# Optimization experiments

Measured on AMD Instinct MI355X. Metric: run time of the kernel, lower is better.

Reference implementation:

```python
import jax, jax.numpy as jnp
import numpy as np

N = 100000      # nodes
E = 1600000     # edges (avg degree 16)
G = 1000        # graphs in batch
F_IN = 128      # num_features
C = 10          # num_classes
EPS = 1e-5


def setup_inputs() -> dict:
    key = jax.random.key(0)
    ks = jax.random.split(key, 12)
    w = lambda k, shape: jax.random.normal(k, shape, jnp.float32) * 0.05
    return {
        'x': jax.random.normal(ks[0], (N, F_IN), jnp.float32),
        'edge_index': jax.random.randint(ks[1], (2, E), 0, N, jnp.int32),
        'edge_weights': jax.random.randint(ks[2], (E,), 0, 2, jnp.int32),
        'batch': jnp.sort(jax.random.randint(ks[3], (N,), 0, G, jnp.int32)),
        'num_graphs': G,
        # initial MLP: Linear(128,32)+BN+ReLU, Linear(32,32)+BN+ReLU
        'W1': w(ks[4], (F_IN, 32)), 'b1': jnp.zeros(32), 'g1': jnp.ones(32), 'bt1': jnp.zeros(32),
        'W2': w(ks[5], (32, 32)), 'b2': jnp.zeros(32), 'g2': jnp.ones(32), 'bt2': jnp.zeros(32),
        'Wl0': w(ks[6], (32, C)), 'bl0': jnp.zeros(C),   # initial_linear
        'Wg1': w(ks[7], (32, 64)), 'bg1': jnp.zeros(64),  # GCNConv 1
        'Wl1': w(ks[8], (64, C)), 'bl1': jnp.zeros(C),
        'Wg2': w(ks[9], (64, 64)), 'bg2': jnp.zeros(64),  # GCNConv 2
        'Wl2': w(ks[10], (64, C)), 'bl2': jnp.zeros(C),
    }


def _bn(h, gamma, beta):
    # BatchNorm1d in training mode: biased batch statistics over nodes
    mu = h.mean(0)
    var = ((h - mu) ** 2).mean(0)
    return gamma * (h - mu) * jax.lax.rsqrt(var + EPS) + beta


def _gcn(h_in, row, col, w, W, b):
    # PyG GCNConv with self-loops: D^{-1/2}(A+I)D^{-1/2} X W + b,
    # edges with mask weight 0 contribute nothing (incl. to degree).
    n = h_in.shape[0]
    h = h_in @ W
    deg = jax.ops.segment_sum(w, col, num_segments=n) + 1.0  # +1 self-loop
    dinv = jax.lax.rsqrt(deg)
    norm = w * dinv[row] * dinv[col]                  # [E]
    agg = jax.ops.segment_sum(h[row] * norm[:, None], col, num_segments=n)
    agg = agg + h * (dinv * dinv)[:, None]            # self-loop term
    return agg + b


def _pool_max(h, batch, num_graphs):
    # torch_scatter scatter_max readout; empty segments -> 0
    p = jax.ops.segment_max(h, batch, num_segments=num_graphs)
    return jnp.where(jnp.isfinite(p), p, 0.0)


def reference(x, edge_index, edge_weights, batch, num_graphs,
              W1, b1, g1, bt1, W2, b2, g2, bt2, Wl0, bl0,
              Wg1, bg1, Wl1, bl1, Wg2, bg2, Wl2, bl2):
    row, col = edge_index[0], edge_index[1]
    w = (edge_weights == 1).astype(x.dtype)  # boolean edge mask as 0/1 weight
    # initial MLP (dropout treated as identity for deterministic reference)
    h = jax.nn.relu(_bn(x @ W1 + b1, g1, bt1))
    h = jax.nn.relu(_bn(h @ W2 + b2, g2, bt2))
    out = _pool_max(h @ Wl0 + bl0, batch, num_graphs)
    # layer 1
    h = _gcn(h, row, col, w, Wg1, bg1)
    out = out + _pool_max(h, batch, num_graphs) @ Wl1 + bl1
    # layer 2
    h = _gcn(h, row, col, w, Wg2, bg2)
    out = out + _pool_max(h, batch, num_graphs) @ Wl2 + bl2
    return out
```

## Files before the change

kernel.cpp:

```cpp
#include <hip/hip_runtime.h>

#define NN 100000
#define EE 1600000
#define GG 1000
#define BN_EPS 1e-5f
#define NTB 782
#define SLOT 64

__device__ __forceinline__ unsigned encf(float f){
  unsigned u = __float_as_uint(f);
  return (u & 0x80000000u) ? ~u : (u | 0x80000000u);
}
__device__ __forceinline__ float dec0(unsigned e){
  unsigned u = (e & 0x80000000u) ? (e & 0x7fffffffu) : ~e;
  float f = __uint_as_float(u);
  return isfinite(f) ? f : 0.0f;
}
__device__ __forceinline__ unsigned short f2bf(float f){
  unsigned u = __float_as_uint(f);
  u += 0x7FFFu + ((u >> 16) & 1u);
  return (unsigned short)(u >> 16);
}
__device__ __forceinline__ float bf2f(unsigned short s){
  return __uint_as_float(((unsigned)s) << 16);
}

#define STEP4(AX, WV) \
  acc[0][0]=fmaf(a0.AX,WV.x,acc[0][0]); acc[0][1]=fmaf(a0.AX,WV.y,acc[0][1]); \
  acc[0][2]=fmaf(a0.AX,WV.z,acc[0][2]); acc[0][3]=fmaf(a0.AX,WV.w,acc[0][3]); \
  acc[1][0]=fmaf(a1.AX,WV.x,acc[1][0]); acc[1][1]=fmaf(a1.AX,WV.y,acc[1][1]); \
  acc[1][2]=fmaf(a1.AX,WV.z,acc[1][2]); acc[1][3]=fmaf(a1.AX,WV.w,acc[1][3]); \
  acc[2][0]=fmaf(a2.AX,WV.x,acc[2][0]); acc[2][1]=fmaf(a2.AX,WV.y,acc[2][1]); \
  acc[2][2]=fmaf(a2.AX,WV.z,acc[2][2]); acc[2][3]=fmaf(a2.AX,WV.w,acc[2][3]); \
  acc[3][0]=fmaf(a3.AX,WV.x,acc[3][0]); acc[3][1]=fmaf(a3.AX,WV.y,acc[3][1]); \
  acc[3][2]=fmaf(a3.AX,WV.z,acc[3][2]); acc[3][3]=fmaf(a3.AX,WV.w,acc[3][3]);

__global__ void k_scatter(const int* __restrict__ ei, const int* __restrict__ ew,
                          int* __restrict__ fill, int* __restrict__ csr,
                          const float* __restrict__ x, unsigned short* __restrict__ Xb){
  const int t = blockIdx.x*256 + threadIdx.x;
  if (t < EE && ew[t] == 1){
    int c = ei[EE + t];
    int pos = atomicAdd(&fill[c], 1);
    if (pos < SLOT) csr[(size_t)c*SLOT + pos] = ei[t];
  }
  const size_t base = (size_t)t * 2;
  #pragma unroll
  for (int i = 0; i < 2; i++){
    const size_t idx = base + i;
    if (idx < (size_t)NN*32){
      float4 v = ((const float4*)x)[idx];
      ushort4 u; u.x=f2bf(v.x); u.y=f2bf(v.y); u.z=f2bf(v.z); u.w=f2bf(v.w);
      ((ushort4*)Xb)[idx] = u;
    }
  }
}

__global__ void k_dinv(const int* __restrict__ fill, float* __restrict__ dinv){
  int i = blockIdx.x*256 + threadIdx.x;
  if (i < NN) dinv[i] = rsqrtf((float)fill[i] + 1.0f);
}

__global__ __launch_bounds__(256) void k_gemm1(const unsigned short* __restrict__ Xb,
    const float* __restrict__ W1, const float* __restrict__ b1,
    unsigned short* __restrict__ Y1b, float* __restrict__ stats){
  __shared__ unsigned short xs[128*136];
  __shared__ unsigned short Ws[128*32];
  __shared__ float red[64];
  const int tid = threadIdx.x;
  if (tid < 64) red[tid] = 0.f;
  #pragma unroll
  for (int j = 0; j < 4; j++){
    int idx = tid + j*256;
    int kk = idx >> 3, cc = idx & 7;
    float4 w = ((const float4*)W1)[(size_t)kk*8 + cc];
    ushort4 u; u.x=f2bf(w.x); u.y=f2bf(w.y); u.z=f2bf(w.z); u.w=f2bf(w.w);
    *(ushort4*)&Ws[kk*32 + cc*4] = u;
  }
  const long rowbase = (long)blockIdx.x*128;
  for (int j = tid; j < 4096; j += 256){
    int rr = j >> 5, kk = j & 31;
    long gr = rowbase + rr;
    ushort4 u = (gr < NN) ? ((const ushort4*)Xb)[gr*32 + kk] : ushort4{0,0,0,0};
    *(ushort4*)&xs[rr*136 + kk*4] = u;
  }
  __syncthreads();
  const int rg = tid >> 3, cg = tid & 7;
  const float4 bv = ((const float4*)b1)[cg];
  float acc[4][4];
  #pragma unroll
  for (int i = 0; i < 4; i++){ acc[i][0]=bv.x; acc[i][1]=bv.y; acc[i][2]=bv.z; acc[i][3]=bv.w; }
  #pragma unroll 4
  for (int k = 0; k < 128; k += 4){
    const ushort4 u0 = *(const ushort4*)&xs[(rg     )*136 + k];
    const ushort4 u1 = *(const ushort4*)&xs[(rg + 32)*136 + k];
    const ushort4 u2 = *(const ushort4*)&xs[(rg + 64)*136 + k];
    const ushort4 u3 = *(const ushort4*)&xs[(rg + 96)*136 + k];
    float4 a0, a1, a2, a3;
    a0.x=bf2f(u0.x); a0.y=bf2f(u0.y); a0.z=bf2f(u0.z); a0.w=bf2f(u0.w);
    a1.x=bf2f(u1.x); a1.y=bf2f(u1.y); a1.z=bf2f(u1.z); a1.w=bf2f(u1.w);
    a2.x=bf2f(u2.x); a2.y=bf2f(u2.y); a2.z=bf2f(u2.z); a2.w=bf2f(u2.w);
    a3.x=bf2f(u3.x); a3.y=bf2f(u3.y); a3.z=bf2f(u3.z); a3.w=bf2f(u3.w);
    const ushort4 wu0 = *(const ushort4*)&Ws[(k+0)*32 + cg*4];
    const ushort4 wu1 = *(const ushort4*)&Ws[(k+1)*32 + cg*4];
    const ushort4 wu2 = *(const ushort4*)&Ws[(k+2)*32 + cg*4];
    const ushort4 wu3 = *(const ushort4*)&Ws[(k+3)*32 + cg*4];
    float4 w0, w1, w2, w3;
    w0.x=bf2f(wu0.x); w0.y=bf2f(wu0.y); w0.z=bf2f(wu0.z); w0.w=bf2f(wu0.w);
    w1.x=bf2f(wu1.x); w1.y=bf2f(wu1.y); w1.z=bf2f(wu1.z); w1.w=bf2f(wu1.w);
    w2.x=bf2f(wu2.x); w2.y=bf2f(wu2.y); w2.z=bf2f(wu2.z); w2.w=bf2f(wu2.w);
    w3.x=bf2f(wu3.x); w3.y=bf2f(wu3.y); w3.z=bf2f(wu3.z); w3.w=bf2f(wu3.w);
    STEP4(x, w0) STEP4(y, w1) STEP4(z, w2) STEP4(w, w3)
  }
  float s[4] = {0,0,0,0}, q[4] = {0,0,0,0};
  #pragma unroll
  for (int i = 0; i < 4; i++){
    const long r = rowbase + rg + 32*i;
    if (r < NN){
      ushort4 o; o.x=f2bf(acc[i][0]); o.y=f2bf(acc[i][1]); o.z=f2bf(acc[i][2]); o.w=f2bf(acc[i][3]);
      ((ushort4*)Y1b)[r*8 + cg] = o;
      #pragma unroll
      for (int j = 0; j < 4; j++){ s[j] += acc[i][j]; q[j] += acc[i][j]*acc[i][j]; }
    }
  }
  __syncthreads();
  #pragma unroll
  for (int j = 0; j < 4; j++){
    atomicAdd(&red[cg*4+j], s[j]);
    atomicAdd(&red[32+cg*4+j], q[j]);
  }
  __syncthreads();
  if (tid < 64) atomicAdd(&stats[tid], red[tid]);
}

__global__ __launch_bounds__(256) void k_mlp2(const unsigned short* __restrict__ Y1b,
    const float* __restrict__ W2, const float* __restrict__ b2,
    const float* __restrict__ g1, const float* __restrict__ bt1,
    float* __restrict__ stats, unsigned short* __restrict__ Y2b){
  __shared__ float ht[128*36];
  __shared__ float Ws[32*32];
  __shared__ float red[64];
  __shared__ float scs[32], shs[32];
  const int tid = threadIdx.x;
  ((float4*)Ws)[tid] = ((const float4*)W2)[tid];
  if (tid < 64) red[tid] = 0.f;
  if (tid < 32){
    float mean = stats[tid] * (1.0f/NN);
    float var  = stats[32 + tid] * (1.0f/NN) - mean*mean;
    float sH = g1[tid] * rsqrtf(fmaxf(var, 0.0f) + BN_EPS);
    scs[tid] = sH; shs[tid] = bt1[tid] - mean*sH;
  }
  __syncthreads();
  const long rowbase = (long)blockIdx.x*128;
  for (int j = tid; j < 1024; j += 256){
    int rr = j >> 3, kk = j & 7;
    long gr = rowbase + rr;
    ushort4 u = (gr < NN) ? ((const ushort4*)Y1b)[gr*8 + kk] : ushort4{0,0,0,0};
    float4 v;
    v.x = fmaxf(fmaf(bf2f(u.x), scs[kk*4+0], shs[kk*4+0]), 0.f);
    v.y = fmaxf(fmaf(bf2f(u.y), scs[kk*4+1], shs[kk*4+1]), 0.f);
    v.z = fmaxf(fmaf(bf2f(u.z), scs[kk*4+2], shs[kk*4+2]), 0.f);
    v.w = fmaxf(fmaf(bf2f(u.w), scs[kk*4+3], shs[kk*4+3]), 0.f);
    *(float4*)&ht[rr*36 + kk*4] = v;
  }
  __syncthreads();
  const int rg = tid >> 3, cg = tid & 7;
  const float4 bv = ((const float4*)b2)[cg];
  float acc[4][4];
  #pragma unroll
  for (int i = 0; i < 4; i++){ acc[i][0]=bv.x; acc[i][1]=bv.y; acc[i][2]=bv.z; acc[i][3]=bv.w; }
  #pragma unroll
  for (int k = 0; k < 32; k += 4){
    const float4 a0 = *(const float4*)&ht[(rg     )*36 + k];
    const float4 a1 = *(const float4*)&ht[(rg + 32)*36 + k];
    const float4 a2 = *(const float4*)&ht[(rg + 64)*36 + k];
    const float4 a3 = *(const float4*)&ht[(rg + 96)*36 + k];
    const float4 w0 = *(const float4*)&Ws[(k+0)*32 + cg*4];
    const float4 w1 = *(const float4*)&Ws[(k+1)*32 + cg*4];
    const float4 w2 = *(const float4*)&Ws[(k+2)*32 + cg*4];
    const float4 w3 = *(const float4*)&Ws[(k+3)*32 + cg*4];
    STEP4(x, w0) STEP4(y, w1) STEP4(z, w2) STEP4(w, w3)
  }
  float s[4] = {0,0,0,0}, q[4] = {0,0,0,0};
  #pragma unroll
  for (int i = 0; i < 4; i++){
    const long r = rowbase + rg + 32*i;
    if (r < NN){
      ushort4 o; o.x=f2bf(acc[i][0]); o.y=f2bf(acc[i][1]); o.z=f2bf(acc[i][2]); o.w=f2bf(acc[i][3]);
      ((ushort4*)Y2b)[r*8 + cg] = o;
      #pragma unroll
      for (int j = 0; j < 4; j++){ s[j] += acc[i][j]; q[j] += acc[i][j]*acc[i][j]; }
    }
  }
  __syncthreads();
  #pragma unroll
  for (int j = 0; j < 4; j++){
    atomicAdd(&red[cg*4+j], s[j]);
    atomicAdd(&red[32+cg*4+j], q[j]);
  }
  __syncthreads();
  if (tid < 64) atomicAdd(&stats[128 + tid], red[tid]);
}

__global__ __launch_bounds__(256) void k_layer0(const unsigned short* __restrict__ Y2b,
    const float* __restrict__ stats, const float* __restrict__ g2,
    const float* __restrict__ bt2, const float* __restrict__ Wg1,
    const float* __restrict__ Wl0, const float* __restrict__ bl0,
    const float* __restrict__ dinv, const int* __restrict__ batch,
    unsigned short* __restrict__ Hs1, unsigned* __restrict__ Pool0){
  __shared__ float hs[32*36];
  __shared__ float Wg[32*64];
  __shared__ float Wl[320];
  __shared__ float bl[10];
  __shared__ float scs[32], shs[32];
  const int tid = threadIdx.x;
  ((float4*)Wg)[tid]       = ((const float4*)Wg1)[tid];
  ((float4*)Wg)[tid + 256] = ((const float4*)Wg1)[tid + 256];
  for (int j = tid; j < 320; j += 256) Wl[j] = Wl0[j];
  if (tid < 10)  bl[tid] = bl0[tid];
  if (tid < 32){
    float mean = stats[128 + tid] * (1.0f/NN);
    float var  = stats[160 + tid] * (1.0f/NN) - mean*mean;
    float s = g2[tid] * rsqrtf(fmaxf(var, 0.0f) + BN_EPS);
    scs[tid] = s; shs[tid] = bt2[tid] - mean*s;
  }
  __syncthreads();
  {
    const int rr = tid >> 3, kk = tid & 7;
    const float4 sc = *(const float4*)&scs[kk*4];
    const float4 sh = *(const float4*)&shs[kk*4];
    ushort4 u = ((const ushort4*)Y2b)[(size_t)blockIdx.x*256 + tid];
    float4 v;
    v.x = fmaxf(fmaf(bf2f(u.x), sc.x, sh.x), 0.f);
    v.y = fmaxf(fmaf(bf2f(u.y), sc.y, sh.y), 0.f);
    v.z = fmaxf(fmaf(bf2f(u.z), sc.z, sh.z), 0.f);
    v.w = fmaxf(fmaf(bf2f(u.w), sc.w, sh.w), 0.f);
    *(float4*)&hs[rr*36 + kk*4] = v;
  }
  __syncthreads();
  const int w = tid >> 6, f = tid & 63;
  for (int i = 0; i < 8; i++){
    const int r = w*8 + i;
    const int row = blockIdx.x*32 + r;
    const float* hr = &hs[r*36];
    float acc = 0.f;
    #pragma unroll
    for (int k = 0; k < 32; k++) acc += hr[k]*Wg[k*64 + f];
    Hs1[(size_t)row*64 + f] = f2bf(acc * dinv[row]);
    if (f < 10){
      float p = bl[f];
      #pragma unroll
      for (int k = 0; k < 32; k++) p += hr[k]*Wl[k*10 + f];
      atomicMax(&Pool0[batch[row]*10 + f], encf(p));
    }
  }
}

__device__ __forceinline__ void gather2(const unsigned short* __restrict__ Hs,
    const int* __restrict__ csr, int sA, int eA, int sB, int eB, int f,
    float& accA, float& accB){
  int jA = sA, jB = sB;
  while (jA + 3 < eA && jB + 3 < eB){
    const int a0 = csr[jA], a1 = csr[jA+1], a2 = csr[jA+2], a3 = csr[jA+3];
    const int b0 = csr[jB], b1 = csr[jB+1], b2 = csr[jB+2], b3 = csr[jB+3];
    float tA0 = bf2f(Hs[(size_t)a0*64 + f]);
    float tA1 = bf2f(Hs[(size_t)a1*64 + f]);
    float tA2 = bf2f(Hs[(size_t)a2*64 + f]);
    float tA3 = bf2f(Hs[(size_t)a3*64 + f]);
    float tB0 = bf2f(Hs[(size_t)b0*64 + f]);
    float tB1 = bf2f(Hs[(size_t)b1*64 + f]);
    float tB2 = bf2f(Hs[(size_t)b2*64 + f]);
    float tB3 = bf2f(Hs[(size_t)b3*64 + f]);
    accA += (tA0 + tA1) + (tA2 + tA3);
    accB += (tB0 + tB1) + (tB2 + tB3);
    jA += 4; jB += 4;
  }
  for (; jA + 3 < eA; jA += 4){
    const int a0 = csr[jA], a1 = csr[jA+1], a2 = csr[jA+2], a3 = csr[jA+3];
    float t0 = bf2f(Hs[(size_t)a0*64 + f]);
    float t1 = bf2f(Hs[(size_t)a1*64 + f]);
    float t2 = bf2f(Hs[(size_t)a2*64 + f]);
    float t3 = bf2f(Hs[(size_t)a3*64 + f]);
    accA += (t0 + t1) + (t2 + t3);
  }
  for (; jB + 3 < eB; jB += 4){
    const int b0 = csr[jB], b1 = csr[jB+1], b2 = csr[jB+2], b3 = csr[jB+3];
    float t0 = bf2f(Hs[(size_t)b0*64 + f]);
    float t1 = bf2f(Hs[(size_t)b1*64 + f]);
    float t2 = bf2f(Hs[(size_t)b2*64 + f]);
    float t3 = bf2f(Hs[(size_t)b3*64 + f]);
    accB += (t0 + t1) + (t2 + t3);
  }
  for (; jA < eA; jA++) accA += bf2f(Hs[(size_t)csr[jA]*64 + f]);
  for (; jB < eB; jB++) accB += bf2f(Hs[(size_t)csr[jB]*64 + f]);
}

__device__ __forceinline__ void pool_epilogue8(float hA, float hB, int w, int f,
    int cA, int cB, const int* __restrict__ batch, unsigned* __restrict__ Pool,
    float (*sm)[64], int* sb){
  sm[w*2][f] = hA; sm[w*2+1][f] = hB;
  if (f == 0){ sb[w*2] = batch[cA]; sb[w*2+1] = batch[cB]; }
  __syncthreads();
  if (w == 0){
    if (sb[0] == sb[7]){
      float m = fmaxf(fmaxf(fmaxf(sm[0][f], sm[1][f]), fmaxf(sm[2][f], sm[3][f])),
                      fmaxf(fmaxf(sm[4][f], sm[5][f]), fmaxf(sm[6][f], sm[7][f])));
      atomicMax(&Pool[sb[0]*64 + f], encf(m));
    } else {
      #pragma unroll
      for (int i = 0; i < 8; i++)
        atomicMax(&Pool[sb[i]*64 + f], encf(sm[i][f]));
    }
  }
}

__global__ __launch_bounds__(256) void k_agg1(const unsigned short* __restrict__ Hs,
    const float* __restrict__ dinv, const int* __restrict__ fill,
    const int* __restrict__ csr, const float* __restrict__ bias,
    const int* __restrict__ batch, unsigned short* __restrict__ H2b,
    unsigned* __restrict__ Pool){
  __shared__ float sm[8][64];
  __shared__ int sb[8];
  const int w = threadIdx.x >> 6, f = threadIdx.x & 63;
  const int cA = blockIdx.x*8 + w*2, cB = cA + 1;
  const int sA = cA*SLOT, nA = min(fill[cA], SLOT);
  const int sB = cB*SLOT, nB = min(fill[cB], SLOT);
  float accA = 0.f, accB = 0.f;
  gather2(Hs, csr, sA, sA + nA, sB, sB + nB, f, accA, accB);
  const float dA = dinv[cA], dB = dinv[cB];
  const float bf = bias[f];
  const float hA = fmaf(accA + bf2f(Hs[(size_t)cA*64 + f]), dA, bf);
  const float hB = fmaf(accB + bf2f(Hs[(size_t)cB*64 + f]), dB, bf);
  H2b[(size_t)cA*64 + f] = f2bf(hA);
  H2b[(size_t)cB*64 + f] = f2bf(hB);
  pool_epilogue8(hA, hB, w, f, cA, cB, batch, Pool, sm, sb);
}

__global__ __launch_bounds__(256) void k_agg2(const unsigned short* __restrict__ Hs,
    const float* __restrict__ dinv, const int* __restrict__ fill,
    const int* __restrict__ csr, const float* __restrict__ bias,
    const int* __restrict__ batch, unsigned* __restrict__ Pool){
  __shared__ float sm[8][64];
  __shared__ int sb[8];
  const int w = threadIdx.x >> 6, f = threadIdx.x & 63;
  const int cA = blockIdx.x*8 + w*2, cB = cA + 1;
  const int sA = cA*SLOT, nA = min(fill[cA], SLOT);
  const int sB = cB*SLOT, nB = min(fill[cB], SLOT);
  float accA = 0.f, accB = 0.f;
  gather2(Hs, csr, sA, sA + nA, sB, sB + nB, f, accA, accB);
  const float dA = dinv[cA], dB = dinv[cB];
  const float bf = bias[f];
  const float hA = fmaf(accA + bf2f(Hs[(size_t)cA*64 + f]), dA, bf);
  const float hB = fmaf(accB + bf2f(Hs[(size_t)cB*64 + f]), dB, bf);
  pool_epilogue8(hA, hB, w, f, cA, cB, batch, Pool, sm, sb);
}

__global__ __launch_bounds__(256) void k_layer1(const unsigned short* __restrict__ H2b,
    const float* __restrict__ Wg2, const float* __restrict__ dinv,
    unsigned short* __restrict__ Hs2){
  __shared__ float as[32*68];
  __shared__ float Wg[64*64];
  const int tid = threadIdx.x;
  #pragma unroll
  for (int j = 0; j < 4; j++) ((float4*)Wg)[tid + j*256] = ((const float4*)Wg2)[tid + j*256];
  {
    const int rr = tid >> 3, kk = tid & 7;
    ushort4 v0 = ((const ushort4*)H2b)[(size_t)blockIdx.x*512 + tid*2];
    ushort4 v1 = ((const ushort4*)H2b)[(size_t)blockIdx.x*512 + tid*2 + 1];
    float* dst = &as[rr*68 + kk*8];
    dst[0]=bf2f(v0.x); dst[1]=bf2f(v0.y); dst[2]=bf2f(v0.z); dst[3]=bf2f(v0.w);
    dst[4]=bf2f(v1.x); dst[5]=bf2f(v1.y); dst[6]=bf2f(v1.z); dst[7]=bf2f(v1.w);
  }
  __syncthreads();
  const int w = tid >> 6, f = tid & 63;
  for (int i = 0; i < 8; i++){
    const int r = w*8 + i;
    const int row = blockIdx.x*32 + r;
    const float* ar = &as[r*68];
    float acc = 0.f;
    #pragma unroll
    for (int k = 0; k < 64; k++) acc += ar[k]*Wg[k*64 + f];
    Hs2[(size_t)row*64 + f] = f2bf(acc * dinv[row]);
  }
}

__global__ __launch_bounds__(256) void k_final(const unsigned* __restrict__ P0,
    const unsigned* __restrict__ P1, const unsigned* __restrict__ P2,
    const float* __restrict__ Wl1, const float* __restrict__ bl1,
    const float* __restrict__ Wl2, const float* __restrict__ bl2,
    float* __restrict__ out){
  const int t = blockIdx.x*256 + threadIdx.x;
  const int g = t >> 4, c = t & 15;
  if (g >= GG || c >= 10) return;
  float acc = dec0(P0[g*10 + c]) + bl1[c] + bl2[c];
  for (int f = 0; f < 64; f++){
    acc += dec0(P1[g*64 + f]) * Wl1[f*10 + c];
    acc += dec0(P2[g*64 + f]) * Wl2[f*10 + c];
  }
  out[g*10 + c] = acc;
}

extern "C" void kernel_launch(void* const* d_in, const int* in_sizes, int n_in,
                              void* d_out, int out_size, void* d_ws, size_t ws_size,
                              hipStream_t stream){
  const float* x   = (const float*)d_in[0];
  const int*   ei  = (const int*)d_in[1];
  const int*   ew  = (const int*)d_in[2];
  const int*   bat = (const int*)d_in[3];
  const float* W1  = (const float*)d_in[5],  *b1  = (const float*)d_in[6];
  const float* g1  = (const float*)d_in[7],  *bt1 = (const float*)d_in[8];
  const float* W2  = (const float*)d_in[9],  *b2  = (const float*)d_in[10];
  const float* g2  = (const float*)d_in[11], *bt2 = (const float*)d_in[12];
  const float* Wl0 = (const float*)d_in[13], *bl0 = (const float*)d_in[14];
  const float* Wg1 = (const float*)d_in[15], *bg1 = (const float*)d_in[16];
  const float* Wl1 = (const float*)d_in[17], *bl1 = (const float*)d_in[18];
  const float* Wg2 = (const float*)d_in[19], *bg2 = (const float*)d_in[20];
  const float* Wl2 = (const float*)d_in[21], *bl2 = (const float*)d_in[22];

  float* ws = (float*)d_ws;
  const size_t oFill  = 0;
  const size_t oStats = NN;
  const size_t oP0    = oStats + 256;
  const size_t oP1    = oP0 + (size_t)GG*10;
  const size_t oP2    = oP1 + (size_t)GG*64;
  const size_t oZEnd  = oP2 + (size_t)GG*64;
  const size_t oDinv  = oZEnd;
  const size_t oCsr   = oDinv + NN;
  const size_t oR1    = oCsr + (size_t)NN*SLOT;
  const size_t oR2    = oR1 + (size_t)NN*16;
  const size_t oR3    = oR2 + (size_t)NN*16;
  const size_t oR4    = oR3 + (size_t)NN*32;

  int*   fill  = (int*)(ws + oFill);
  float* stats = ws + oStats;
  unsigned* P0 = (unsigned*)(ws + oP0);
  unsigned* P1 = (unsigned*)(ws + oP1);
  unsigned* P2 = (unsigned*)(ws + oP2);
  float* dinv  = ws + oDinv;
  int*   csr   = (int*)(ws + oCsr);
  unsigned short* Y1b = (unsigned short*)(ws + oR1);
  unsigned short* Y2b = (unsigned short*)(ws + oR2);
  unsigned short* Xb  = (unsigned short*)(ws + oR3);
  unsigned short* Hs1 = (unsigned short*)(ws + oR3);
  unsigned short* Hs2 = (unsigned short*)(ws + oR3);
  unsigned short* H2b = (unsigned short*)(ws + oR4);

  (void)hipMemsetAsync(d_ws, 0, oZEnd*sizeof(float), stream);

  k_scatter<<<EE/256, 256, 0, stream>>>(ei, ew, fill, csr, x, Xb);
  k_dinv   <<<(NN + 255)/256, 256, 0, stream>>>(fill, dinv);
  k_gemm1<<<NTB, 256, 0, stream>>>(Xb, W1, b1, Y1b, stats);
  k_mlp2 <<<NTB, 256, 0, stream>>>(Y1b, W2, b2, g1, bt1, stats, Y2b);
  k_layer0<<<3125, 256, 0, stream>>>(Y2b, stats, g2, bt2, Wg1, Wl0, bl0, dinv, bat, Hs1, P0);
  k_agg1 <<<NN/8, 256, 0, stream>>>(Hs1, dinv, fill, csr, bg1, bat, H2b, P1);
  k_layer1<<<3125, 256, 0, stream>>>(H2b, Wg2, dinv, Hs2);
  k_agg2 <<<NN/8, 256, 0, stream>>>(Hs2, dinv, fill, csr, bg2, bat, P2);
  k_final<<<(GG*16 + 255)/256, 256, 0, stream>>>(P0, P1, P2, Wl1, bl1, Wl2, bl2, (float*)d_out);
}
```

Before: 283.0 us.

## Window edge scatter by destination range and compute dinv inline from fill

The edge scatter now launches 8 block groups per 256-edge chunk. Each group only handles edges whose destination falls in one eighth of the node range, so the atomics and CSR writes of concurrently running blocks land in a narrower, more cache-friendly address window. The separate k_dinv kernel and its buffer are removed, and each consumer recomputes rsqrt(fill+1) on the fly, saving a launch and a pass. The cost is that every block rereads the column indices, so edge-index reads rise eightfold and the launch has many more blocks.

```diff
diff --git a/kernel.cpp b/kernel.cpp
--- a/kernel.cpp
+++ b/kernel.cpp
@@ -6,6 +6,8 @@
 #define BN_EPS 1e-5f
 #define NTB 782
 #define SLOT 64
+#define WND 12500
+#define NCH 6250
 
 __device__ __forceinline__ unsigned encf(float f){
   unsigned u = __float_as_uint(f);
@@ -38,27 +40,26 @@
 __global__ void k_scatter(const int* __restrict__ ei, const int* __restrict__ ew,
                           int* __restrict__ fill, int* __restrict__ csr,
                           const float* __restrict__ x, unsigned short* __restrict__ Xb){
-  const int t = blockIdx.x*256 + threadIdx.x;
-  if (t < EE && ew[t] == 1){
-    int c = ei[EE + t];
-    int pos = atomicAdd(&fill[c], 1);
-    if (pos < SLOT) csr[(size_t)c*SLOT + pos] = ei[t];
-  }
-  const size_t base = (size_t)t * 2;
-  #pragma unroll
-  for (int i = 0; i < 2; i++){
-    const size_t idx = base + i;
-    if (idx < (size_t)NN*32){
-      float4 v = ((const float4*)x)[idx];
-      ushort4 u; u.x=f2bf(v.x); u.y=f2bf(v.y); u.z=f2bf(v.z); u.w=f2bf(v.w);
-      ((ushort4*)Xb)[idx] = u;
+  const int w = blockIdx.x & 7;
+  const int chunk = blockIdx.x >> 3;
+  const int e = chunk*256 + threadIdx.x;
+  const int col = ei[EE + e];
+  if (col / WND == w && ew[e] == 1){
+    int pos = atomicAdd(&fill[col], 1);
+    if (pos < SLOT) csr[(size_t)col*SLOT + pos] = ei[e];
+  }
+  if (w == 7){
+    const size_t base = ((size_t)chunk*256 + threadIdx.x) * 2;
+    #pragma unroll
+    for (int i = 0; i < 2; i++){
+      const size_t idx = base + i;
+      if (idx < (size_t)NN*32){
+        float4 v = ((const float4*)x)[idx];
+        ushort4 u; u.x=f2bf(v.x); u.y=f2bf(v.y); u.z=f2bf(v.z); u.w=f2bf(v.w);
+        ((ushort4*)Xb)[idx] = u;
+      }
     }
   }
-}
-
-__global__ void k_dinv(const int* __restrict__ fill, float* __restrict__ dinv){
-  int i = blockIdx.x*256 + threadIdx.x;
-  if (i < NN) dinv[i] = rsqrtf((float)fill[i] + 1.0f);
 }
 
 __global__ __launch_bounds__(256) void k_gemm1(const unsigned short* __restrict__ Xb,
@@ -206,7 +207,7 @@
     const float* __restrict__ stats, const float* __restrict__ g2,
     const float* __restrict__ bt2, const float* __restrict__ Wg1,
     const float* __restrict__ Wl0, const float* __restrict__ bl0,
-    const float* __restrict__ dinv, const int* __restrict__ batch,
+    const int* __restrict__ fill, const int* __restrict__ batch,
     unsigned short* __restrict__ Hs1, unsigned* __restrict__ Pool0){
   __shared__ float hs[32*36];
   __shared__ float Wg[32*64];
@@ -246,7 +247,8 @@
     float acc = 0.f;
     #pragma unroll
     for (int k = 0; k < 32; k++) acc += hr[k]*Wg[k*64 + f];
-    Hs1[(size_t)row*64 + f] = f2bf(acc * dinv[row]);
+    const float dv = rsqrtf((float)fill[row] + 1.0f);
+    Hs1[(size_t)row*64 + f] = f2bf(acc * dv);
     if (f < 10){
       float p = bl[f];
       #pragma unroll
@@ -315,19 +317,19 @@
 }
 
 __global__ __launch_bounds__(256) void k_agg1(const unsigned short* __restrict__ Hs,
-    const float* __restrict__ dinv, const int* __restrict__ fill,
-    const int* __restrict__ csr, const float* __restrict__ bias,
-    const int* __restrict__ batch, unsigned short* __restrict__ H2b,
-    unsigned* __restrict__ Pool){
+    const int* __restrict__ fill, const int* __restrict__ csr,
+    const float* __restrict__ bias, const int* __restrict__ batch,
+    unsigned short* __restrict__ H2b, unsigned* __restrict__ Pool){
   __shared__ float sm[8][64];
   __shared__ int sb[8];
   const int w = threadIdx.x >> 6, f = threadIdx.x & 63;
   const int cA = blockIdx.x*8 + w*2, cB = cA + 1;
-  const int sA = cA*SLOT, nA = min(fill[cA], SLOT);
-  const int sB = cB*SLOT, nB = min(fill[cB], SLOT);
+  const int fA = fill[cA], fB = fill[cB];
+  const int sA = cA*SLOT, nA = min(fA, SLOT);
+  const int sB = cB*SLOT, nB = min(fB, SLOT);
   float accA = 0.f, accB = 0.f;
   gather2(Hs, csr, sA, sA + nA, sB, sB + nB, f, accA, accB);
-  const float dA = dinv[cA], dB = dinv[cB];
+  const float dA = rsqrtf((float)fA + 1.0f), dB = rsqrtf((float)fB + 1.0f);
   const float bf = bias[f];
   const float hA = fmaf(accA + bf2f(Hs[(size_t)cA*64 + f]), dA, bf);
   const float hB = fmaf(accB + bf2f(Hs[(size_t)cB*64 + f]), dB, bf);
@@ -337,18 +339,19 @@
 }
 
 __global__ __launch_bounds__(256) void k_agg2(const unsigned short* __restrict__ Hs,
-    const float* __restrict__ dinv, const int* __restrict__ fill,
-    const int* __restrict__ csr, const float* __restrict__ bias,
-    const int* __restrict__ batch, unsigned* __restrict__ Pool){
+    const int* __restrict__ fill, const int* __restrict__ csr,
+    const float* __restrict__ bias, const int* __restrict__ batch,
+    unsigned* __restrict__ Pool){
   __shared__ float sm[8][64];
   __shared__ int sb[8];
   const int w = threadIdx.x >> 6, f = threadIdx.x & 63;
   const int cA = blockIdx.x*8 + w*2, cB = cA + 1;
-  const int sA = cA*SLOT, nA = min(fill[cA], SLOT);
-  const int sB = cB*SLOT, nB = min(fill[cB], SLOT);
+  const int fA = fill[cA], fB = fill[cB];
+  const int sA = cA*SLOT, nA = min(fA, SLOT);
+  const int sB = cB*SLOT, nB = min(fB, SLOT);
   float accA = 0.f, accB = 0.f;
   gather2(Hs, csr, sA, sA + nA, sB, sB + nB, f, accA, accB);
-  const float dA = dinv[cA], dB = dinv[cB];
+  const float dA = rsqrtf((float)fA + 1.0f), dB = rsqrtf((float)fB + 1.0f);
   const float bf = bias[f];
   const float hA = fmaf(accA + bf2f(Hs[(size_t)cA*64 + f]), dA, bf);
   const float hB = fmaf(accB + bf2f(Hs[(size_t)cB*64 + f]), dB, bf);
@@ -356,7 +359,7 @@
 }
 
 __global__ __launch_bounds__(256) void k_layer1(const unsigned short* __restrict__ H2b,
-    const float* __restrict__ Wg2, const float* __restrict__ dinv,
+    const float* __restrict__ Wg2, const int* __restrict__ fill,
     unsigned short* __restrict__ Hs2){
   __shared__ float as[32*68];
   __shared__ float Wg[64*64];
@@ -380,7 +383,7 @@
     float acc = 0.f;
     #pragma unroll
     for (int k = 0; k < 64; k++) acc += ar[k]*Wg[k*64 + f];
-    Hs2[(size_t)row*64 + f] = f2bf(acc * dinv[row]);
+    Hs2[(size_t)row*64 + f] = f2bf(acc * rsqrtf((float)fill[row] + 1.0f));
   }
 }
 
@@ -424,8 +427,7 @@
   const size_t oP1    = oP0 + (size_t)GG*10;
   const size_t oP2    = oP1 + (size_t)GG*64;
   const size_t oZEnd  = oP2 + (size_t)GG*64;
-  const size_t oDinv  = oZEnd;
-  const size_t oCsr   = oDinv + NN;
+  const size_t oCsr   = oZEnd;
   const size_t oR1    = oCsr + (size_t)NN*SLOT;
   const size_t oR2    = oR1 + (size_t)NN*16;
   const size_t oR3    = oR2 + (size_t)NN*16;
@@ -436,7 +438,6 @@
   unsigned* P0 = (unsigned*)(ws + oP0);
   unsigned* P1 = (unsigned*)(ws + oP1);
   unsigned* P2 = (unsigned*)(ws + oP2);
-  float* dinv  = ws + oDinv;
   int*   csr   = (int*)(ws + oCsr);
   unsigned short* Y1b = (unsigned short*)(ws + oR1);
   unsigned short* Y2b = (unsigned short*)(ws + oR2);
@@ -447,13 +448,12 @@
 
   (void)hipMemsetAsync(d_ws, 0, oZEnd*sizeof(float), stream);
 
-  k_scatter<<<EE/256, 256, 0, stream>>>(ei, ew, fill, csr, x, Xb);
-  k_dinv   <<<(NN + 255)/256, 256, 0, stream>>>(fill, dinv);
+  k_scatter<<<NCH*8, 256, 0, stream>>>(ei, ew, fill, csr, x, Xb);
   k_gemm1<<<NTB, 256, 0, stream>>>(Xb, W1, b1, Y1b, stats);
   k_mlp2 <<<NTB, 256, 0, stream>>>(Y1b, W2, b2, g1, bt1, stats, Y2b);
-  k_layer0<<<3125, 256, 0, stream>>>(Y2b, stats, g2, bt2, Wg1, Wl0, bl0, dinv, bat, Hs1, P0);
-  k_agg1 <<<NN/8, 256, 0, stream>>>(Hs1, dinv, fill, csr, bg1, bat, H2b, P1);
-  k_layer1<<<3125, 256, 0, stream>>>(H2b, Wg2, dinv, Hs2);
-  k_agg2 <<<NN/8, 256, 0, stream>>>(Hs2, dinv, fill, csr, bg2, bat, P2);
+  k_layer0<<<3125, 256, 0, stream>>>(Y2b, stats, g2, bt2, Wg1, Wl0, bl0, fill, bat, Hs1, P0);
+  k_agg1 <<<NN/8, 256, 0, stream>>>(Hs1, fill, csr, bg1, bat, H2b, P1);
+  k_layer1<<<3125, 256, 0, stream>>>(H2b, Wg2, fill, Hs2);
+  k_agg2 <<<NN/8, 256, 0, stream>>>(Hs2, fill, csr, bg2, bat, P2);
   k_final<<<(GG*16 + 255)/256, 256, 0, stream>>>(P0, P1, P2, Wl1, bl1, Wl2, bl2, (float*)d_out);
 }
```

New measurement: 322.3 us. 1.14x slower.
